# Kernel optimization log

Measured on AMD Instinct MI355X. Metric: run time of the kernel, lower is better.

The kernel has to match this reference:

```python
import jax, jax.numpy as jnp
import numpy as np

NEG_SLOPE = 0.2  # PyG GATConv default negative_slope
EPS = 1e-16      # PyG softmax denominator epsilon


def gat_conv(x, W, att_src, att_dst, bias, src, dst, num_nodes, concat):
    H, C = att_src.shape
    h = (x @ W).reshape(-1, H, C)                    # [N,H,C]
    a_src = jnp.einsum('nhc,hc->nh', h, att_src)      # [N,H]
    a_dst = jnp.einsum('nhc,hc->nh', h, att_dst)      # [N,H]
    e = a_src[src] + a_dst[dst]                       # [E,H]
    e = jax.nn.leaky_relu(e, NEG_SLOPE)
    # segment softmax over incoming edges of each destination node
    e_max = jax.ops.segment_max(e, dst, num_segments=num_nodes)   # [N,H]
    e_max = jnp.where(jnp.isfinite(e_max), e_max, 0.0)
    p = jnp.exp(e - e_max[dst])                        # [E,H]
    denom = jax.ops.segment_sum(p, dst, num_segments=num_nodes)   # [N,H]
    alpha = p / (denom[dst] + EPS)                     # [E,H]
    msg = h[src] * alpha[:, :, None]                   # [E,H,C]
    out = jax.ops.segment_sum(msg, dst, num_segments=num_nodes)   # [N,H,C]
    if concat:
        out = out.reshape(num_nodes, H * C)
    else:
        out = out.mean(axis=1)
    return out + bias


def setup_inputs() -> dict:
    key = jax.random.key(0)
    ks = jax.random.split(key, 10)
    N, E, Fin, H, C, OUT = 50000, 400000, 128, 8, 32, 32
    s = 0.05
    return {
        'x': jax.random.normal(ks[0], (N, Fin), jnp.float32),
        'edge_index': jax.random.randint(ks[1], (2, E), 0, N, jnp.int64),
        'W1': jax.random.normal(ks[2], (Fin, H * C), jnp.float32) * s,
        'att_src1': jax.random.normal(ks[3], (H, C), jnp.float32) * s,
        'att_dst1': jax.random.normal(ks[4], (H, C), jnp.float32) * s,
        'b1': jax.random.normal(ks[5], (H * C,), jnp.float32) * s,
        'W2': jax.random.normal(ks[6], (H * C, H * OUT), jnp.float32) * s,
        'att_src2': jax.random.normal(ks[7], (H, OUT), jnp.float32) * s,
        'att_dst2': jax.random.normal(ks[8], (H, OUT), jnp.float32) * s,
        'b2': jax.random.normal(ks[9], (OUT,), jnp.float32) * s,
    }


def reference(x, edge_index, W1, att_src1, att_dst1, b1, W2, att_src2, att_dst2, b2):
    N = x.shape[0]
    src, dst = edge_index[0], edge_index[1]
    h = gat_conv(x, W1, att_src1, att_dst1, b1, src, dst, N, concat=True)
    h = jax.nn.elu(h)  # dropout p=0 / eval: identity
    out = gat_conv(h, W2, att_src2, att_dst2, b2, src, dst, N, concat=False)
    return out
```

## Files before the change

kernel.cpp:

```cpp
#include <hip/hip_runtime.h>
#include <math.h>

#define NEG_SLOPE 0.2f

typedef float f32x4 __attribute__((ext_vector_type(4)));
typedef short bf16x8 __attribute__((ext_vector_type(8)));
typedef unsigned short ushortv8 __attribute__((ext_vector_type(8)));

__device__ __forceinline__ unsigned short f2bf(float f) {
    union { float f; unsigned u; } uu; uu.f = f;
    unsigned r = uu.u + 0x7FFF + ((uu.u >> 16) & 1);
    return (unsigned short)(r >> 16);
}
__device__ __forceinline__ float bf2f(unsigned short u) {
    union { unsigned u; float f; } x; x.u = ((unsigned)u) << 16; return x.f;
}

__global__ void prep_kernel(const float* __restrict__ W1, unsigned short* __restrict__ Wt1,
                            const float* __restrict__ W2, unsigned short* __restrict__ Wt2,
                            int* __restrict__ counts, int* __restrict__ cursor, int N)
{
    int u = blockIdx.x * 256 + threadIdx.x;
    if (u < 32768) {
        int nn = u >> 7, k = u & 127;
        Wt1[u] = f2bf(W1[(size_t)k * 256 + nn]);
        return;
    }
    u -= 32768;
    if (u < 65536) {
        int nn = u >> 8, k = u & 255;
        Wt2[u] = f2bf(W2[(size_t)k * 256 + nn]);
        return;
    }
    u -= 65536;
    if (u < N) { counts[u] = 0; cursor[u] = 0; }
}

__global__ void hist_kernel(const int* __restrict__ dst, int* __restrict__ counts, int E)
{
    int e = blockIdx.x * 256 + threadIdx.x;
    if (e < E) atomicAdd(&counts[dst[e]], 1);
}

template<int CVT>
__global__ __launch_bounds__(512) void gemm_mfma(
    const void* __restrict__ Av,
    const unsigned short* __restrict__ Bt,
    unsigned short* __restrict__ C,
    const float* __restrict__ att_s,
    const float* __restrict__ att_d,
    float* __restrict__ a_s,
    float* __restrict__ a_d,
    int M, int K)
{
    __shared__ unsigned short As[128 * 64];
    __shared__ unsigned short Bs[256 * 64];
    const int tid  = threadIdx.x;
    const int lane = tid & 63;
    const int wave = tid >> 6;
    const int wr = wave >> 2, wc = wave & 3;
    const int row0 = blockIdx.x * 128;

    f32x4 acc[4][4] = {};

    for (int k0 = 0; k0 < K; k0 += 64) {
        ushortv8 va[2], vb[4];
        #pragma unroll
        for (int i = 0; i < 2; ++i) {
            int c  = i * 512 + tid;
            int r  = c >> 3, cc = c & 7;
            int ga = row0 + r; if (ga >= M) ga = M - 1;
            if constexpr (CVT) {
                const float* ap = (const float*)Av + (size_t)ga * K + k0 + cc * 8;
                float4 lo = *(const float4*)ap;
                float4 hi = *(const float4*)(ap + 4);
                ushortv8 o;
                o[0]=f2bf(lo.x); o[1]=f2bf(lo.y); o[2]=f2bf(lo.z); o[3]=f2bf(lo.w);
                o[4]=f2bf(hi.x); o[5]=f2bf(hi.y); o[6]=f2bf(hi.z); o[7]=f2bf(hi.w);
                va[i] = o;
            } else {
                va[i] = *(const ushortv8*)((const unsigned short*)Av +
                                           (size_t)ga * K + k0 + cc * 8);
            }
        }
        #pragma unroll
        for (int i = 0; i < 4; ++i) {
            int c  = i * 512 + tid;
            int r  = c >> 3, cc = c & 7;
            vb[i] = *(const ushortv8*)(Bt + (size_t)r * K + k0 + cc * 8);
        }
        __syncthreads();
        #pragma unroll
        for (int i = 0; i < 2; ++i) {
            int c  = i * 512 + tid;
            int r  = c >> 3, cc = c & 7;
            *(ushortv8*)(As + r * 64 + (cc ^ (r & 7)) * 8) = va[i];
        }
        #pragma unroll
        for (int i = 0; i < 4; ++i) {
            int c  = i * 512 + tid;
            int r  = c >> 3, cc = c & 7;
            *(ushortv8*)(Bs + r * 64 + (cc ^ (r & 7)) * 8) = vb[i];
        }
        __syncthreads();

        #pragma unroll
        for (int kk = 0; kk < 2; ++kk) {
            const int kbyte = kk * 64 + ((lane >> 4) << 4);
            bf16x8 af[4], bfr[4];
            #pragma unroll
            for (int m = 0; m < 4; ++m) {
                int r = wr * 64 + m * 16 + (lane & 15);
                af[m] = *(const bf16x8*)((const char*)As + r * 128 + (kbyte ^ ((r & 7) << 4)));
            }
            #pragma unroll
            for (int n = 0; n < 4; ++n) {
                int r = wc * 64 + n * 16 + (lane & 15);
                bfr[n] = *(const bf16x8*)((const char*)Bs + r * 128 + (kbyte ^ ((r & 7) << 4)));
            }
            #pragma unroll
            for (int m = 0; m < 4; ++m)
                #pragma unroll
                for (int n = 0; n < 4; ++n)
                    acc[m][n] = __builtin_amdgcn_mfma_f32_16x16x32_bf16(
                        af[m], bfr[n], acc[m][n], 0, 0, 0);
        }
        __syncthreads();
    }

    #pragma unroll
    for (int m = 0; m < 4; ++m) {
        int rbase = row0 + wr * 64 + m * 16 + ((lane >> 4) << 2);
        #pragma unroll
        for (int j = 0; j < 4; ++j) {
            int grow = rbase + j;
            if (grow < M) {
                #pragma unroll
                for (int n = 0; n < 4; ++n)
                    C[(size_t)grow * 256 + wc * 64 + n * 16 + (lane & 15)] =
                        f2bf(acc[m][n][j]);
            }
        }
    }

    float asv[4], adv[4];
    #pragma unroll
    for (int n = 0; n < 4; ++n) {
        int colg = wc * 64 + n * 16 + (lane & 15);
        asv[n] = att_s[colg];
        adv[n] = att_d[colg];
    }
    const int hbase = wc * 2;
    #pragma unroll
    for (int m = 0; m < 4; ++m) {
        int rbase = row0 + wr * 64 + m * 16 + ((lane >> 4) << 2);
        #pragma unroll
        for (int j = 0; j < 4; ++j) {
            int grow = rbase + j;
            #pragma unroll
            for (int t = 0; t < 2; ++t) {
                float vs = acc[m][2*t][j] * asv[2*t] + acc[m][2*t+1][j] * asv[2*t+1];
                float vd = acc[m][2*t][j] * adv[2*t] + acc[m][2*t+1][j] * adv[2*t+1];
                #pragma unroll
                for (int off = 1; off < 16; off <<= 1) {
                    vs += __shfl_xor(vs, off);
                    vd += __shfl_xor(vd, off);
                }
                if ((lane & 15) == 0 && grow < M) {
                    a_s[(size_t)grow * 8 + hbase + t] = vs;
                    a_d[(size_t)grow * 8 + hbase + t] = vd;
                }
            }
        }
    }
}

__global__ __launch_bounds__(256) void scan_blk(
    const int* __restrict__ counts, int* __restrict__ incl, int* __restrict__ bsum, int N)
{
    __shared__ int wtot[4], wexc[4];
    int t = blockIdx.x * 256 + threadIdx.x;
    int lane = threadIdx.x & 63, wid = threadIdx.x >> 6;
    int v = (t < N) ? counts[t] : 0;
    int s = v;
    #pragma unroll
    for (int off = 1; off < 64; off <<= 1) {
        int u = __shfl_up(s, off);
        if (lane >= off) s += u;
    }
    if (lane == 63) wtot[wid] = s;
    __syncthreads();
    if (threadIdx.x == 0) {
        int r = 0;
        #pragma unroll
        for (int w = 0; w < 4; ++w) { wexc[w] = r; r += wtot[w]; }
    }
    __syncthreads();
    int out = s + wexc[wid];
    if (t < N) incl[t] = out;
    if (threadIdx.x == 255) bsum[blockIdx.x] = out;
}

__global__ __launch_bounds__(256) void scan_top(int* __restrict__ bsum, int nb)
{
    __shared__ int wtot[4], wexc[4];
    int tid = threadIdx.x;
    int lane = tid & 63, wid = tid >> 6;
    int v = (tid < nb) ? bsum[tid] : 0;
    int s = v;
    #pragma unroll
    for (int off = 1; off < 64; off <<= 1) {
        int u = __shfl_up(s, off);
        if (lane >= off) s += u;
    }
    if (lane == 63) wtot[wid] = s;
    __syncthreads();
    if (tid == 0) {
        int r = 0;
        #pragma unroll
        for (int w = 0; w < 4; ++w) { wexc[w] = r; r += wtot[w]; }
    }
    __syncthreads();
    if (tid < nb) bsum[tid] = s + wexc[wid] - v;
}

__global__ void fill_kernel(const int* __restrict__ src, const int* __restrict__ dst,
                            const int* __restrict__ incl, const int* __restrict__ bsum,
                            int* __restrict__ rowptr, int* __restrict__ cursor,
                            int* __restrict__ esrc, int N, int E)
{
    int t = blockIdx.x * 256 + threadIdx.x;
    if (t < N) {
        rowptr[t + 1] = incl[t] + bsum[t >> 8];
        if (t == 0) rowptr[0] = 0;
    }
    if (t < E) {
        int d = dst[t];
        int rp = bsum[d >> 8] + ((d & 255) ? incl[d - 1] : 0);
        int pos = rp + atomicAdd(&cursor[d], 1);
        esrc[pos] = src[t];
    }
}

template<int LAYER>
__global__ __launch_bounds__(128) void gat_agg(
    const unsigned short* __restrict__ h, const float* __restrict__ a_s,
    const float* __restrict__ a_d, const int* __restrict__ rowptr,
    const int* __restrict__ esrc, const float* __restrict__ bias,
    float* __restrict__ out, unsigned short* __restrict__ out_b, int N)
{
    const int n  = blockIdx.x * 4 + (threadIdx.x >> 5);
    if (n >= N) return;
    const int sl   = threadIdx.x & 31;
    const int head = sl >> 2;
    const int beg = rowptr[n];
    const int deg = rowptr[n + 1] - beg;

    const float adn = a_d[(size_t)n*8 + head];
    float dsum = 0.f;
    float2 acc2[4] = {{0.f,0.f},{0.f,0.f},{0.f,0.f},{0.f,0.f}};

    int j0 = 0;
    for (; j0 + 4 <= deg; j0 += 4) {
        int s0 = esrc[beg + j0 + 0];
        int s1 = esrc[beg + j0 + 1];
        int s2 = esrc[beg + j0 + 2];
        int s3 = esrc[beg + j0 + 3];
        int sv[4] = {s0, s1, s2, s3};
        #pragma unroll
        for (int k = 0; k < 4; ++k) {
            int s = sv[k];
            float e = a_s[(size_t)s*8 + head] + adn;
            e = fmaxf(e, NEG_SLOPE * e);
            float p = __expf(e);
            dsum += p;
            uint4 hv = *(const uint4*)(h + (size_t)s*256 + sl*8);
            const unsigned* hw = (const unsigned*)&hv;
            #pragma unroll
            for (int i = 0; i < 4; ++i) {
                acc2[i].x += p * __uint_as_float(hw[i] << 16);
                acc2[i].y += p * __uint_as_float(hw[i] & 0xffff0000u);
            }
        }
    }
    for (; j0 < deg; ++j0) {
        int s = esrc[beg + j0];
        float e = a_s[(size_t)s*8 + head] + adn;
        e = fmaxf(e, NEG_SLOPE * e);
        float p = __expf(e);
        dsum += p;
        uint4 hv = *(const uint4*)(h + (size_t)s*256 + sl*8);
        const unsigned* hw = (const unsigned*)&hv;
        #pragma unroll
        for (int i = 0; i < 4; ++i) {
            acc2[i].x += p * __uint_as_float(hw[i] << 16);
            acc2[i].y += p * __uint_as_float(hw[i] & 0xffff0000u);
        }
    }

    float invd = 1.f / (dsum + 1e-16f);

    if (LAYER == 1) {
        ushortv8 o;
        #pragma unroll
        for (int i = 0; i < 4; ++i) {
            float v0 = acc2[i].x * invd + bias[sl*8 + 2*i];
            float v1 = acc2[i].y * invd + bias[sl*8 + 2*i + 1];
            o[2*i]   = f2bf(v0 > 0.f ? v0 : expf(v0) - 1.f);
            o[2*i+1] = f2bf(v1 > 0.f ? v1 : expf(v1) - 1.f);
        }
        *(ushortv8*)(out_b + (size_t)n*256 + sl*8) = o;
    } else {
        #pragma unroll
        for (int i = 0; i < 4; ++i) { acc2[i].x *= invd; acc2[i].y *= invd; }
        #pragma unroll
        for (int m = 4; m <= 16; m <<= 1)
            #pragma unroll
            for (int i = 0; i < 4; ++i) {
                acc2[i].x += __shfl_xor(acc2[i].x, m);
                acc2[i].y += __shfl_xor(acc2[i].y, m);
            }
        if (sl < 4) {
            float4 lo = make_float4(acc2[0].x*0.125f + bias[sl*8+0],
                                    acc2[0].y*0.125f + bias[sl*8+1],
                                    acc2[1].x*0.125f + bias[sl*8+2],
                                    acc2[1].y*0.125f + bias[sl*8+3]);
            float4 hi = make_float4(acc2[2].x*0.125f + bias[sl*8+4],
                                    acc2[2].y*0.125f + bias[sl*8+5],
                                    acc2[3].x*0.125f + bias[sl*8+6],
                                    acc2[3].y*0.125f + bias[sl*8+7]);
            *(float4*)(out + (size_t)n*32 + sl*8)     = lo;
            *(float4*)(out + (size_t)n*32 + sl*8 + 4) = hi;
        }
    }
}

extern "C" void kernel_launch(void* const* d_in, const int* in_sizes, int n_in,
                              void* d_out, int out_size, void* d_ws, size_t ws_size,
                              hipStream_t stream)
{
    const float* x   = (const float*)d_in[0];
    const int*   ei  = (const int*)  d_in[1];
    const float* W1  = (const float*)d_in[2];
    const float* as1 = (const float*)d_in[3];
    const float* ad1 = (const float*)d_in[4];
    const float* b1  = (const float*)d_in[5];
    const float* W2  = (const float*)d_in[6];
    const float* as2 = (const float*)d_in[7];
    const float* ad2 = (const float*)d_in[8];
    const float* b2  = (const float*)d_in[9];

    const int N = in_sizes[0] / 128;
    const int E = in_sizes[1] / 2;
    const int* srcp = ei;
    const int* dstp = ei + E;

    char* ws = (char*)d_ws;
    unsigned short* hb    = (unsigned short*)ws;  ws += (size_t)N * 256 * 2;
    unsigned short* out1b = (unsigned short*)ws;  ws += (size_t)N * 256 * 2;
    unsigned short* Wt1   = (unsigned short*)ws;  ws += 256 * 128 * 2;
    unsigned short* Wt2   = (unsigned short*)ws;  ws += 256 * 256 * 2;
    float*          a_s   = (float*)ws;           ws += (size_t)N * 8 * 4;
    float*          a_d   = (float*)ws;           ws += (size_t)N * 8 * 4;
    int*            counts= (int*)ws;             ws += (size_t)N * 4;
    int*            cursor= (int*)ws;             ws += (size_t)N * 4;
    int*            incl  = (int*)ws;             ws += (size_t)N * 4;
    int*            bsum  = (int*)ws;             ws += 256 * 4;
    int*            rowptr= (int*)ws;             ws += (size_t)(N + 1) * 4;
    int*            esrc  = (int*)ws;

    const int nb = (N + 255) / 256;

    {
        int tot = 32768 + 65536 + N;
        prep_kernel<<<(tot + 255) / 256, 256, 0, stream>>>(
            W1, Wt1, W2, Wt2, counts, cursor, N);
    }
    hist_kernel<<<(E + 255) / 256, 256, 0, stream>>>(dstp, counts, E);
    scan_blk<<<nb, 256, 0, stream>>>(counts, incl, bsum, N);
    scan_top<<<1, 256, 0, stream>>>(bsum, nb);
    fill_kernel<<<(E + 255) / 256, 256, 0, stream>>>(srcp, dstp, incl, bsum,
                                                     rowptr, cursor, esrc, N, E);

    const int gridM = (N + 127) / 128;

    gemm_mfma<1><<<gridM, 512, 0, stream>>>(x, Wt1, hb, as1, ad1,
                                            a_s, a_d, N, 128);
    gat_agg<1><<<(N + 3) / 4, 128, 0, stream>>>(hb, a_s, a_d, rowptr, esrc, b1,
                                                nullptr, out1b, N);

    gemm_mfma<0><<<gridM, 512, 0, stream>>>(out1b, Wt2, hb, as2, ad2,
                                            a_s, a_d, N, 256);
    gat_agg<2><<<(N + 3) / 4, 128, 0, stream>>>(hb, a_s, a_d, rowptr, esrc, b2,
                                                (float*)d_out, nullptr, N);
}
```

Before: 176.0 us.

## Fuse CSR fill into first GEMM launch and register-prefetch next K tile

The CSR fill step (rowptr and esrc scatter) is folded into the first GEMM launch as extra blocks, so it runs alongside the layer-1 GEMM and one kernel launch is dropped. The GEMM main loop now loads the next K tile into registers while MFMAs run on the current tile, and the trailing barrier is removed. This adds register pressure and makes fill blocks share launch bounds and LDS allocation with GEMM blocks.

After: 170.3 us. -3.2%, faster.

```diff
diff --git a/kernel.cpp b/kernel.cpp
--- a/kernel.cpp
+++ b/kernel.cpp
@@ -51,10 +51,31 @@
     const float* __restrict__ att_d,
     float* __restrict__ a_s,
     float* __restrict__ a_d,
-    int M, int K)
+    int M, int K, int gemmBlocks,
+    const int* __restrict__ srcp, const int* __restrict__ dstp,
+    const int* __restrict__ incl, const int* __restrict__ bsum,
+    int* __restrict__ rowptr, int* __restrict__ cursor,
+    int* __restrict__ esrc, int E)
 {
     __shared__ unsigned short As[128 * 64];
     __shared__ unsigned short Bs[256 * 64];
+
+    if ((int)blockIdx.x >= gemmBlocks) {
+        int t = ((int)blockIdx.x - gemmBlocks) * 512 + threadIdx.x;
+        int Nn = M;
+        if (t < Nn) {
+            rowptr[t + 1] = incl[t] + bsum[t >> 8];
+            if (t == 0) rowptr[0] = 0;
+        }
+        if (t < E) {
+            int d = dstp[t];
+            int rp = bsum[d >> 8] + ((d & 255) ? incl[d - 1] : 0);
+            int pos = rp + atomicAdd(&cursor[d], 1);
+            esrc[pos] = srcp[t];
+        }
+        return;
+    }
+
     const int tid  = threadIdx.x;
     const int lane = tid & 63;
     const int wave = tid >> 6;
@@ -62,9 +83,9 @@
     const int row0 = blockIdx.x * 128;
 
     f32x4 acc[4][4] = {};
-
-    for (int k0 = 0; k0 < K; k0 += 64) {
-        ushortv8 va[2], vb[4];
+    ushortv8 va[2], vb[4];
+
+    auto load_tile = [&](int k0) {
         #pragma unroll
         for (int i = 0; i < 2; ++i) {
             int c  = i * 512 + tid;
@@ -89,6 +110,11 @@
             int r  = c >> 3, cc = c & 7;
             vb[i] = *(const ushortv8*)(Bt + (size_t)r * K + k0 + cc * 8);
         }
+    };
+
+    load_tile(0);
+
+    for (int k0 = 0; k0 < K; k0 += 64) {
         __syncthreads();
         #pragma unroll
         for (int i = 0; i < 2; ++i) {
@@ -104,6 +130,7 @@
         }
         __syncthreads();
 
+        if (k0 + 64 < K) load_tile(k0 + 64);
         #pragma unroll
         for (int kk = 0; kk < 2; ++kk) {
             const int kbyte = kk * 64 + ((lane >> 4) << 4);
@@ -125,7 +152,6 @@
                     acc[m][n] = __builtin_amdgcn_mfma_f32_16x16x32_bf16(
                         af[m], bfr[n], acc[m][n], 0, 0, 0);
         }
-        __syncthreads();
     }
 
     #pragma unroll
@@ -222,24 +248,6 @@
     }
     __syncthreads();
     if (tid < nb) bsum[tid] = s + wexc[wid] - v;
-}
-
-__global__ void fill_kernel(const int* __restrict__ src, const int* __restrict__ dst,
-                            const int* __restrict__ incl, const int* __restrict__ bsum,
-                            int* __restrict__ rowptr, int* __restrict__ cursor,
-                            int* __restrict__ esrc, int N, int E)
-{
-    int t = blockIdx.x * 256 + threadIdx.x;
-    if (t < N) {
-        rowptr[t + 1] = incl[t] + bsum[t >> 8];
-        if (t == 0) rowptr[0] = 0;
-    }
-    if (t < E) {
-        int d = dst[t];
-        int rp = bsum[d >> 8] + ((d & 255) ? incl[d - 1] : 0);
-        int pos = rp + atomicAdd(&cursor[d], 1);
-        esrc[pos] = src[t];
-    }
 }
 
 template<int LAYER>
@@ -379,18 +387,19 @@
     hist_kernel<<<(E + 255) / 256, 256, 0, stream>>>(dstp, counts, E);
     scan_blk<<<nb, 256, 0, stream>>>(counts, incl, bsum, N);
     scan_top<<<1, 256, 0, stream>>>(bsum, nb);
-    fill_kernel<<<(E + 255) / 256, 256, 0, stream>>>(srcp, dstp, incl, bsum,
-                                                     rowptr, cursor, esrc, N, E);
 
     const int gridM = (N + 127) / 128;
-
-    gemm_mfma<1><<<gridM, 512, 0, stream>>>(x, Wt1, hb, as1, ad1,
-                                            a_s, a_d, N, 128);
+    const int fillB = (E + 511) / 512;
+
+    gemm_mfma<1><<<gridM + fillB, 512, 0, stream>>>(
+        x, Wt1, hb, as1, ad1, a_s, a_d, N, 128, gridM,
+        srcp, dstp, incl, bsum, rowptr, cursor, esrc, E);
     gat_agg<1><<<(N + 3) / 4, 128, 0, stream>>>(hb, a_s, a_d, rowptr, esrc, b1,
                                                 nullptr, out1b, N);
 
-    gemm_mfma<0><<<gridM, 512, 0, stream>>>(out1b, Wt2, hb, as2, ad2,
-                                            a_s, a_d, N, 256);
+    gemm_mfma<0><<<gridM, 512, 0, stream>>>(
+        out1b, Wt2, hb, as2, ad2, a_s, a_d, N, 256, gridM,
+        srcp, dstp, incl, bsum, rowptr, cursor, esrc, E);
     gat_agg<2><<<(N + 3) / 4, 128, 0, stream>>>(hb, a_s, a_d, rowptr, esrc, b2,
                                                 (float*)d_out, nullptr, N);
 }
```
